# Optimization experiments

Hardware: AMD Instinct MI355X
Metric: run time of the kernel (lower is better)

## Reference

```python
import jax, jax.numpy as jnp
import numpy as np

DIM = 1024        # model dim
HEADS = 1         # num_heads (fc1 in_features==1 forces this)
HDIM = DIM // HEADS
INNER = 16        # dim_inner
B, L = 2, 4096
ROPE_BASE = 32.0


def _apply_rope(x, pos, base):
    # x: [b, l, h, d]; standard rotate-half RoPE
    d = x.shape[-1]
    inv_freq = base ** (-jnp.arange(0, d, 2, dtype=jnp.float32) / d)   # [d/2]
    ang = pos[:, None].astype(jnp.float32) * inv_freq                  # [l, d/2]
    emb = jnp.concatenate([ang, ang], axis=-1)                         # [l, d]
    cos = jnp.cos(emb)[None, :, None, :].astype(x.dtype)
    sin = jnp.sin(emb)[None, :, None, :].astype(x.dtype)
    x1, x2 = x[..., : d // 2], x[..., d // 2:]
    rot = jnp.concatenate([-x2, x1], axis=-1)
    return x * cos + rot * sin


def setup_inputs() -> dict:
    key = jax.random.key(0)
    ks = jax.random.split(key, 7)
    hidden_states = jax.random.normal(ks[0], (B, L, DIM), dtype=jnp.float32)
    Wq = jax.random.normal(ks[1], (DIM, DIM), dtype=jnp.float32) * 0.02
    Wk = jax.random.normal(ks[2], (DIM, DIM), dtype=jnp.float32) * 0.02
    fc1_w = jax.random.normal(ks[3], (INNER, 1), dtype=jnp.float32) * 0.1
    fc1_b = jax.random.normal(ks[4], (INNER,), dtype=jnp.float32) * 0.1
    fc2_w = jax.random.normal(ks[5], (DIM, INNER), dtype=jnp.float32) * 0.1
    fc2_b = jax.random.normal(ks[6], (DIM,), dtype=jnp.float32) * 0.1
    return {"hidden_states": hidden_states, "Wq": Wq, "Wk": Wk,
            "fc1_w": fc1_w, "fc1_b": fc1_b, "fc2_w": fc2_w, "fc2_b": fc2_b}


def reference(hidden_states, Wq, Wk, fc1_w, fc1_b, fc2_w, fc2_b):
    b, l, _ = hidden_states.shape
    # projections, cast to bf16 as in the torch module
    q = (hidden_states @ Wq.T).reshape(b, l, HEADS, HDIM).astype(jnp.bfloat16)
    k = (hidden_states @ Wk.T).reshape(b, l, HEADS, HDIM).astype(jnp.bfloat16)
    pos = jnp.arange(l)
    q = _apply_rope(q, pos, ROPE_BASE)
    k = _apply_rope(k, pos, ROPE_BASE)
    # causal exp(QK) with NO softmax normalization; accumulate in fp32
    scores = jnp.einsum('bqhd,bkhd->bhqk',
                        q.astype(jnp.float32), k.astype(jnp.float32)) / (HDIM ** 0.5)
    causal = jnp.tril(jnp.ones((l, l), dtype=bool))                    # [l, l]
    exp_qk = jnp.where(causal[None, None], jnp.exp(scores), 0.0)       # [b, h, l, l]
    o = jnp.swapaxes(exp_qk.sum(axis=-1), 1, 2)                        # [b, l, h]
    # small MLP: h(=1) -> INNER -> DIM
    o = jax.nn.relu(o @ fc1_w.T + fc1_b)
    return o @ fc2_w.T + fc2_b                                         # [b, l, DIM]
```

## Files before the change

kernel.cpp:

```cpp
#include <hip/hip_runtime.h>
#include <hip/hip_bf16.h>

typedef __bf16 bf16_t;
typedef __bf16 bf16x4 __attribute__((ext_vector_type(4)));
typedef __bf16 bf16x8 __attribute__((ext_vector_type(8)));
typedef float f32x4 __attribute__((ext_vector_type(4)));

#define B_   2
#define L_   4096
#define DIM_ 1024
#define M_   (B_ * L_)
#define NTASK2_ 272

__device__ __forceinline__ void ld_g2l_16(const bf16_t* g, bf16_t* l) {
  __builtin_amdgcn_global_load_lds(
      (__attribute__((address_space(1))) void*)g,
      (__attribute__((address_space(3))) void*)l, 16, 0, 0);
}

__global__ void cvt_all(const float* __restrict__ hs, const float* __restrict__ wq,
                        const float* __restrict__ wk, bf16_t* __restrict__ hs_b,
                        bf16_t* __restrict__ wq_b, bf16_t* __restrict__ wk_b,
                        float* __restrict__ o) {
  const int N_HS = M_ * DIM_ / 4, N_W = DIM_ * DIM_ / 4;
  int i = blockIdx.x * blockDim.x + threadIdx.x;
  if (i < M_ / 4) ((float4*)o)[i] = float4{0.f, 0.f, 0.f, 0.f};
  const float* s; bf16_t* d; int idx;
  if (i < N_HS)            { s = hs; d = hs_b; idx = i; }
  else if (i < N_HS + N_W) { s = wq; d = wq_b; idx = i - N_HS; }
  else                     { s = wk; d = wk_b; idx = i - N_HS - N_W; }
  float4 v = ((const float4*)s)[idx];
  bf16x4 ov = { (bf16_t)v.x, (bf16_t)v.y, (bf16_t)v.z, (bf16_t)v.w };
  ((bf16x4*)d)[idx] = ov;
}

template <int BSEGS>
__device__ __forceinline__ void core256(const bf16_t* __restrict__ A,
                                        const bf16_t* __restrict__ B0,
                                        const bf16_t* __restrict__ B1,
                                        bf16_t* sm, bool active,
                                        f32x4 (&acc)[4][BSEGS / 2]) {
  constexpr int SEGS = 16 + BSEGS;
  constexpr int BUF  = SEGS * 512;
  const int tid  = threadIdx.x;
  const int wave = tid >> 6, lane = tid & 63;
  const int wm = wave >> 1, wn = wave & 1;
  const int quad = lane >> 4, l16 = lane & 15;
  const int srow = lane >> 2;
  const int scol = (((lane & 3) ^ ((lane >> 3) & 3)) * 8);
  const int rsw  = ((l16 >> 1) & 3) * 8;
  const int loff = l16 * 32 + ((quad * 8) ^ rsw);

  const bf16_t* gA0 = A + (size_t)(wave * 16 + srow) * DIM_ + scol;
  const bf16_t* gA1 = A + (size_t)((wave + 8) * 16 + srow) * DIM_ + scol;
  const bf16_t* gB0 = B0 + (size_t)(wave * 16 + srow) * DIM_ + scol;
  const bf16_t* gB1 = gB0;
  if constexpr (BSEGS == 16) gB1 = B1 + (size_t)(wave * 16 + srow) * DIM_ + scol;

  bf16_t* p0 = sm;
  bf16_t* p1 = sm + BUF;
  bf16_t* p2 = sm + 2 * BUF;

  auto stage = [&](int kk, bf16_t* buf) {
    ld_g2l_16(gA0 + kk, buf + wave * 512);
    ld_g2l_16(gA1 + kk, buf + (wave + 8) * 512);
    ld_g2l_16(gB0 + kk, buf + (16 + wave) * 512);
    if constexpr (BSEGS == 16) ld_g2l_16(gB1 + kk, buf + (24 + wave) * 512);
  };

  stage(0, p0);
  stage(32, p1);
  if constexpr (BSEGS == 16) asm volatile("s_waitcnt vmcnt(4)" ::: "memory");
  else                       asm volatile("s_waitcnt vmcnt(3)" ::: "memory");
  __builtin_amdgcn_s_barrier();

  for (int s = 0; s < 32; ++s) {
    bf16x8 aF[4], bF[BSEGS / 2];
    if (active) {
#pragma unroll
      for (int rf = 0; rf < 4; ++rf)
        aF[rf] = *(const bf16x8*)(p0 + (wm * 4 + rf) * 512 + loff);
#pragma unroll
      for (int cf = 0; cf < BSEGS / 2; ++cf) {
        int k = (cf & 3) + wn * 4 + (cf >> 2) * 8;
        bF[cf] = *(const bf16x8*)(p0 + (16 + k) * 512 + loff);
      }
    }
    if (s < 30) stage((s + 2) * 32, p2);
    asm volatile("s_waitcnt lgkmcnt(0)" ::: "memory");
    __builtin_amdgcn_sched_barrier(0);
    if (active) {
      __builtin_amdgcn_s_setprio(1);
#pragma unroll
      for (int rf = 0; rf < 4; ++rf)
#pragma unroll
        for (int cf = 0; cf < BSEGS / 2; ++cf)
          acc[rf][cf] = __builtin_amdgcn_mfma_f32_16x16x32_bf16(
              aF[rf], bF[cf], acc[rf][cf], 0, 0, 0);
      __builtin_amdgcn_s_setprio(0);
    }
    if (s < 30) {
      if constexpr (BSEGS == 16) asm volatile("s_waitcnt vmcnt(4)" ::: "memory");
      else                       asm volatile("s_waitcnt vmcnt(3)" ::: "memory");
    } else if (s == 30) {
      asm volatile("s_waitcnt vmcnt(0)" ::: "memory");
    }
    __builtin_amdgcn_s_barrier();
    bf16_t* t0 = p0; p0 = p1; p1 = p2; p2 = t0;
  }
}

__global__ __launch_bounds__(512, 2)
void proj_gemm(const bf16_t* __restrict__ A, const bf16_t* __restrict__ Wqb,
               const bf16_t* __restrict__ Wkb, bf16_t* __restrict__ Cq,
               bf16_t* __restrict__ Ck) {
  __shared__ __attribute__((aligned(16))) bf16_t sm[3 * 32 * 512];
  const int bid = blockIdx.x;
  const int xcd = bid & 7, slot = bid >> 3;
  const int m0 = (xcd * 4 + (slot >> 3)) * 256;
  const int zn = slot & 7;
  const int z = zn >> 2, n0 = (zn & 3) * 128;
  const bf16_t* Wb = z ? Wkb : Wqb;
  bf16_t* Cm = z ? Ck : Cq;

  f32x4 acc[4][8] = {};
  core256<16>(A + (size_t)m0 * DIM_, Wb + (size_t)n0 * DIM_,
              Wb + (size_t)(n0 + 512) * DIM_, sm, true, acc);

  const int tid = threadIdx.x, wave = tid >> 6, lane = tid & 63;
  const int wm = wave >> 1, wn = wave & 1;
  const int quad = lane >> 4, l16 = lane & 15;

  float inv[4];
#pragma unroll
  for (int cf = 0; cf < 4; ++cf) {
    int j = n0 + wn * 64 + cf * 16 + l16;
    inv[cf] = exp2f((float)j * (-5.0f / 512.0f));
  }

#pragma unroll 1
  for (int g = 0; g < 2; ++g) {
    __syncthreads();
#pragma unroll
    for (int rf = 0; rf < 4; ++rf)
#pragma unroll
      for (int r = 0; r < 4; ++r) {
        int row = wm * 64 + rf * 16 + quad * 4 + r;
        float posf = (float)((m0 + row) & (L_ - 1));
#pragma unroll
        for (int cf = 0; cf < 4; ++cf) {
          int col = wn * 64 + cf * 16 + l16;
          float ang = posf * inv[cf];
          float c = cosf(ang), s = sinf(ang);
          float cb = (float)(bf16_t)c, sb = (float)(bf16_t)s;
          float x1 = (float)(bf16_t)acc[rf][cf][r];
          float x2 = (float)(bf16_t)acc[rf][cf + 4][r];
          float v = g ? (x2 * cb + x1 * sb) : (x1 * cb - x2 * sb);
          sm[row * 136 + col] = (bf16_t)v;
        }
      }
    __syncthreads();
#pragma unroll
    for (int it = 0; it < 8; ++it) {
      int row = it * 32 + (tid >> 4);
      int c8  = (tid & 15) * 8;
      bf16x8 v = *(const bf16x8*)(sm + row * 136 + c8);
      *(bf16x8*)(Cm + (size_t)(m0 + row) * DIM_ + n0 + g * 512 + c8) = v;
    }
  }
}

__global__ __launch_bounds__(512, 2)
void attn_rowsum(const bf16_t* __restrict__ Q, const bf16_t* __restrict__ Kc,
                 float* __restrict__ o) {
  __shared__ __attribute__((aligned(16))) bf16_t sm[3 * 24 * 512];
  int logical = (blockIdx.x & 7) * 68 + (blockIdx.x >> 3);
  int b = logical / NTASK2_;
  int t = logical - b * NTASK2_;
  int mi = (int)((sqrtf(4.0f * (float)t + 1.0f) - 1.0f) * 0.5f);
  while ((mi + 1) * (mi + 2) <= t) ++mi;
  while (mi * (mi + 1) > t) --mi;
  int nt = t - mi * (mi + 1);

  const int tid = threadIdx.x, wave = tid >> 6, lane = tid & 63;
  const int wm = wave >> 1, wn = wave & 1;
  const int quad = lane >> 4, l16 = lane & 15;

  const bf16_t* A  = Q  + (size_t)b * L_ * DIM_ + (size_t)mi * 256 * DIM_;
  const bf16_t* Bp = Kc + (size_t)b * L_ * DIM_ + (size_t)nt * 128 * DIM_;

  bool active = (mi * 256 + wm * 64 + 63) >= nt * 128;

  f32x4 acc[4][4] = {};
  core256<8>(A, Bp, nullptr, sm, active, acc);

  if (active) {
    const bool masked = (nt >= 2 * mi);
#pragma unroll
    for (int rf = 0; rf < 4; ++rf) {
#pragma unroll
      for (int r = 0; r < 4; ++r) {
        int grow = mi * 256 + wm * 64 + rf * 16 + quad * 4 + r;
        float sum = 0.0f;
#pragma unroll
        for (int cf = 0; cf < 4; ++cf) {
          int gcol = nt * 128 + wn * 64 + cf * 16 + l16;
          float e = __expf(acc[rf][cf][r] * 0.03125f);
          if (!masked || gcol <= grow) sum += e;
        }
        sum += __shfl_xor(sum, 1);
        sum += __shfl_xor(sum, 2);
        sum += __shfl_xor(sum, 4);
        sum += __shfl_xor(sum, 8);
        if (l16 == 0)
          atomicAdd(&o[b * L_ + grow], sum);
      }
    }
  }
}

__global__ __launch_bounds__(256)
void mlp_out_kernel(const float* __restrict__ o, const float* __restrict__ fc1_w,
                    const float* __restrict__ fc1_b, const float* __restrict__ fc2_w,
                    const float* __restrict__ fc2_b, float* __restrict__ out) {
  const int R = 16;
  int row0 = blockIdx.x * R;
  int tid = threadIdx.x;
  __shared__ float h[R][16];
  {
    int rl = tid >> 4, i = tid & 15;
    float s = o[row0 + rl];
    h[rl][i] = fmaxf(fc1_w[i] * s + fc1_b[i], 0.0f);
  }
  __syncthreads();
  int d = tid * 4;
  float w[4][16];
#pragma unroll
  for (int c = 0; c < 4; ++c)
#pragma unroll
    for (int i = 0; i < 16; ++i) w[c][i] = fc2_w[(d + c) * 16 + i];
  float4 bb = *(const float4*)(fc2_b + d);
  for (int rl = 0; rl < R; ++rl) {
    float4 v = bb;
#pragma unroll
    for (int i = 0; i < 16; ++i) {
      float hv = h[rl][i];
      v.x += w[0][i] * hv; v.y += w[1][i] * hv;
      v.z += w[2][i] * hv; v.w += w[3][i] * hv;
    }
    *(float4*)(out + (size_t)(row0 + rl) * DIM_ + d) = v;
  }
}

extern "C" void kernel_launch(void* const* d_in, const int* in_sizes, int n_in,
                              void* d_out, int out_size, void* d_ws, size_t ws_size,
                              hipStream_t stream) {
  const float* hs    = (const float*)d_in[0];
  const float* Wq    = (const float*)d_in[1];
  const float* Wk    = (const float*)d_in[2];
  const float* fc1_w = (const float*)d_in[3];
  const float* fc1_b = (const float*)d_in[4];
  const float* fc2_w = (const float*)d_in[5];
  const float* fc2_b = (const float*)d_in[6];
  float* out = (float*)d_out;

  char* ws = (char*)d_ws;
  bf16_t* hs_bf = (bf16_t*)ws; ws += (size_t)M_ * DIM_ * 2;
  bf16_t* wq_bf = (bf16_t*)ws; ws += (size_t)DIM_ * DIM_ * 2;
  bf16_t* wk_bf = (bf16_t*)ws; ws += (size_t)DIM_ * DIM_ * 2;
  bf16_t* q_bf  = (bf16_t*)ws; ws += (size_t)M_ * DIM_ * 2;
  bf16_t* k_bf  = (bf16_t*)ws; ws += (size_t)M_ * DIM_ * 2;
  float*  o     = (float*)ws;

  const int n4 = (M_ * DIM_ + 2 * DIM_ * DIM_) / 4;
  cvt_all<<<n4 / 256, 256, 0, stream>>>(hs, Wq, Wk, hs_bf, wq_bf, wk_bf, o);

  proj_gemm<<<256, 512, 0, stream>>>(hs_bf, wq_bf, wk_bf, q_bf, k_bf);

  attn_rowsum<<<544, 512, 0, stream>>>(q_bf, k_bf, o);

  mlp_out_kernel<<<M_ / 16, 256, 0, stream>>>(o, fc1_w, fc1_b, fc2_w, fc2_b, out);
}
```

Before: 280.7 us.

## Split RoPE into separate kernel and retile projection and attention GEMMs

The projection GEMM drops its fused RoPE epilogue and the paired-column 256x256 tiles. It now uses plain 256x128 tiles on a 3D grid and writes results directly with scalar bf16 stores. A new rope_kernel reads Q and K back, applies the rotation and rewrites them in place. The attention row-sum kernel moves from 256x128 to 256x256 tiles (272 blocks instead of 544), masking only on diagonal tiles. The trade is an extra memory round trip for RoPE, uncoalesced stores and no XCD-aware block placement in the projection, against fewer, larger attention tiles.

```diff
diff --git a/kernel.cpp b/kernel.cpp
--- a/kernel.cpp
+++ b/kernel.cpp
@@ -10,7 +10,6 @@
 #define L_   4096
 #define DIM_ 1024
 #define M_   (B_ * L_)
-#define NTASK2_ 272
 
 __device__ __forceinline__ void ld_g2l_16(const bf16_t* g, bf16_t* l) {
   __builtin_amdgcn_global_load_lds(
@@ -114,107 +113,98 @@
 void proj_gemm(const bf16_t* __restrict__ A, const bf16_t* __restrict__ Wqb,
                const bf16_t* __restrict__ Wkb, bf16_t* __restrict__ Cq,
                bf16_t* __restrict__ Ck) {
-  __shared__ __attribute__((aligned(16))) bf16_t sm[3 * 32 * 512];
-  const int bid = blockIdx.x;
-  const int xcd = bid & 7, slot = bid >> 3;
-  const int m0 = (xcd * 4 + (slot >> 3)) * 256;
-  const int zn = slot & 7;
-  const int z = zn >> 2, n0 = (zn & 3) * 128;
-  const bf16_t* Wb = z ? Wkb : Wqb;
-  bf16_t* Cm = z ? Ck : Cq;
-
-  f32x4 acc[4][8] = {};
-  core256<16>(A + (size_t)m0 * DIM_, Wb + (size_t)n0 * DIM_,
-              Wb + (size_t)(n0 + 512) * DIM_, sm, true, acc);
+  __shared__ __attribute__((aligned(16))) bf16_t sm[3 * 24 * 512];
+  const bf16_t* Bm = (blockIdx.z == 0) ? Wqb : Wkb;
+  bf16_t* Cm = (blockIdx.z == 0) ? Cq : Ck;
+  const int m0 = blockIdx.y * 256, n0 = blockIdx.x * 128;
+
+  f32x4 acc[4][4] = {};
+  core256<8>(A + (size_t)m0 * DIM_, Bm + (size_t)n0 * DIM_, nullptr, sm, true,
+             acc);
 
   const int tid = threadIdx.x, wave = tid >> 6, lane = tid & 63;
   const int wm = wave >> 1, wn = wave & 1;
   const int quad = lane >> 4, l16 = lane & 15;
-
-  float inv[4];
-#pragma unroll
-  for (int cf = 0; cf < 4; ++cf) {
-    int j = n0 + wn * 64 + cf * 16 + l16;
-    inv[cf] = exp2f((float)j * (-5.0f / 512.0f));
-  }
-
-#pragma unroll 1
-  for (int g = 0; g < 2; ++g) {
-    __syncthreads();
-#pragma unroll
-    for (int rf = 0; rf < 4; ++rf)
+#pragma unroll
+  for (int rf = 0; rf < 4; ++rf)
+#pragma unroll
+    for (int cf = 0; cf < 4; ++cf) {
+      int k = (cf & 3) + wn * 4;
 #pragma unroll
       for (int r = 0; r < 4; ++r) {
-        int row = wm * 64 + rf * 16 + quad * 4 + r;
-        float posf = (float)((m0 + row) & (L_ - 1));
-#pragma unroll
-        for (int cf = 0; cf < 4; ++cf) {
-          int col = wn * 64 + cf * 16 + l16;
-          float ang = posf * inv[cf];
-          float c = cosf(ang), s = sinf(ang);
-          float cb = (float)(bf16_t)c, sb = (float)(bf16_t)s;
-          float x1 = (float)(bf16_t)acc[rf][cf][r];
-          float x2 = (float)(bf16_t)acc[rf][cf + 4][r];
-          float v = g ? (x2 * cb + x1 * sb) : (x1 * cb - x2 * sb);
-          sm[row * 136 + col] = (bf16_t)v;
-        }
+        int m = m0 + wm * 64 + rf * 16 + quad * 4 + r;
+        int n = n0 + k * 16 + l16;
+        Cm[(size_t)m * DIM_ + n] = (bf16_t)acc[rf][cf][r];
       }
-    __syncthreads();
-#pragma unroll
-    for (int it = 0; it < 8; ++it) {
-      int row = it * 32 + (tid >> 4);
-      int c8  = (tid & 15) * 8;
-      bf16x8 v = *(const bf16x8*)(sm + row * 136 + c8);
-      *(bf16x8*)(Cm + (size_t)(m0 + row) * DIM_ + n0 + g * 512 + c8) = v;
-    }
-  }
+    }
+}
+
+__global__ void rope_kernel(bf16_t* __restrict__ q, bf16_t* __restrict__ k) {
+  bf16_t* x = blockIdx.y ? k : q;
+  int row = blockIdx.x * 2 + (threadIdx.x >> 7);
+  int j0  = (threadIdx.x & 127) * 4;
+  int pos = row & (L_ - 1);
+  bf16_t* p = x + (size_t)row * DIM_;
+  bf16x4 v1 = *(const bf16x4*)(p + j0);
+  bf16x4 v2 = *(const bf16x4*)(p + j0 + 512);
+  bf16x4 o1, o2;
+#pragma unroll
+  for (int u = 0; u < 4; ++u) {
+    int j = j0 + u;
+    float ang = (float)pos * exp2f((float)j * (-5.0f / 512.0f));
+    float c = cosf(ang), s = sinf(ang);
+    float cb = (float)(bf16_t)c, sb = (float)(bf16_t)s;
+    float x1 = (float)v1[u], x2 = (float)v2[u];
+    o1[u] = (bf16_t)(x1 * cb - x2 * sb);
+    o2[u] = (bf16_t)(x2 * cb + x1 * sb);
+  }
+  *(bf16x4*)(p + j0) = o1;
+  *(bf16x4*)(p + j0 + 512) = o2;
 }
 
 __global__ __launch_bounds__(512, 2)
 void attn_rowsum(const bf16_t* __restrict__ Q, const bf16_t* __restrict__ Kc,
                  float* __restrict__ o) {
-  __shared__ __attribute__((aligned(16))) bf16_t sm[3 * 24 * 512];
-  int logical = (blockIdx.x & 7) * 68 + (blockIdx.x >> 3);
-  int b = logical / NTASK2_;
-  int t = logical - b * NTASK2_;
-  int mi = (int)((sqrtf(4.0f * (float)t + 1.0f) - 1.0f) * 0.5f);
-  while ((mi + 1) * (mi + 2) <= t) ++mi;
-  while (mi * (mi + 1) > t) --mi;
-  int nt = t - mi * (mi + 1);
+  __shared__ __attribute__((aligned(16))) bf16_t sm[3 * 32 * 512];
+  int logical = (blockIdx.x & 7) * 34 + (blockIdx.x >> 3);
+  int b = (logical >= 136) ? 1 : 0;
+  int t = logical - b * 136;
+  int mi = (int)((sqrtf(8.0f * (float)t + 1.0f) - 1.0f) * 0.5f);
+  while ((mi + 1) * (mi + 2) / 2 <= t) ++mi;
+  while (mi * (mi + 1) / 2 > t) --mi;
+  int ntt = t - mi * (mi + 1) / 2;
 
   const int tid = threadIdx.x, wave = tid >> 6, lane = tid & 63;
   const int wm = wave >> 1, wn = wave & 1;
   const int quad = lane >> 4, l16 = lane & 15;
 
   const bf16_t* A  = Q  + (size_t)b * L_ * DIM_ + (size_t)mi * 256 * DIM_;
-  const bf16_t* Bp = Kc + (size_t)b * L_ * DIM_ + (size_t)nt * 128 * DIM_;
-
-  bool active = (mi * 256 + wm * 64 + 63) >= nt * 128;
-
-  f32x4 acc[4][4] = {};
-  core256<8>(A, Bp, nullptr, sm, active, acc);
-
-  if (active) {
-    const bool masked = (nt >= 2 * mi);
-#pragma unroll
-    for (int rf = 0; rf < 4; ++rf) {
-#pragma unroll
-      for (int r = 0; r < 4; ++r) {
-        int grow = mi * 256 + wm * 64 + rf * 16 + quad * 4 + r;
-        float sum = 0.0f;
-#pragma unroll
-        for (int cf = 0; cf < 4; ++cf) {
-          int gcol = nt * 128 + wn * 64 + cf * 16 + l16;
-          float e = __expf(acc[rf][cf][r] * 0.03125f);
-          if (!masked || gcol <= grow) sum += e;
-        }
-        sum += __shfl_xor(sum, 1);
-        sum += __shfl_xor(sum, 2);
-        sum += __shfl_xor(sum, 4);
-        sum += __shfl_xor(sum, 8);
-        if (l16 == 0)
-          atomicAdd(&o[b * L_ + grow], sum);
+  const bf16_t* B0 = Kc + (size_t)b * L_ * DIM_ + (size_t)ntt * 256 * DIM_;
+  const bf16_t* B1 = B0 + (size_t)128 * DIM_;
+
+  f32x4 acc[4][8] = {};
+  core256<16>(A, B0, B1, sm, true, acc);
+
+  const bool diag = (ntt == mi);
+#pragma unroll
+  for (int rf = 0; rf < 4; ++rf) {
+#pragma unroll
+    for (int r = 0; r < 4; ++r) {
+      int grow = mi * 256 + wm * 64 + rf * 16 + quad * 4 + r;
+      float sum = 0.0f;
+#pragma unroll
+      for (int cf = 0; cf < 8; ++cf) {
+        int k = (cf & 3) + wn * 4 + (cf >> 2) * 8;
+        int gcol = ntt * 256 + k * 16 + l16;
+        float e = __expf(acc[rf][cf][r] * 0.03125f);
+        if (!diag || gcol <= grow) sum += e;
       }
+      sum += __shfl_xor(sum, 1);
+      sum += __shfl_xor(sum, 2);
+      sum += __shfl_xor(sum, 4);
+      sum += __shfl_xor(sum, 8);
+      if (l16 == 0)
+        atomicAdd(&o[b * L_ + grow], sum);
     }
   }
 }
@@ -275,9 +265,13 @@
   const int n4 = (M_ * DIM_ + 2 * DIM_ * DIM_) / 4;
   cvt_all<<<n4 / 256, 256, 0, stream>>>(hs, Wq, Wk, hs_bf, wq_bf, wk_bf, o);
 
-  proj_gemm<<<256, 512, 0, stream>>>(hs_bf, wq_bf, wk_bf, q_bf, k_bf);
-
-  attn_rowsum<<<544, 512, 0, stream>>>(q_bf, k_bf, o);
+  dim3 gg(DIM_ / 128, M_ / 256, 2);
+  proj_gemm<<<gg, 512, 0, stream>>>(hs_bf, wq_bf, wk_bf, q_bf, k_bf);
+
+  dim3 gr(M_ / 2, 2);
+  rope_kernel<<<gr, 256, 0, stream>>>(q_bf, k_bf);
+
+  attn_rowsum<<<272, 512, 0, stream>>>(q_bf, k_bf, o);
 
   mlp_out_kernel<<<M_ / 16, 256, 0, stream>>>(o, fc1_w, fc1_b, fc2_w, fc2_b, out);
 }
```

After: 243.1 us. 1.15x faster.
